# Performance work log

Measured on AMD Instinct MI355X. Metric: run time of the kernel, lower is better.

Reference implementation:

```python
import jax, jax.numpy as jnp
import numpy as np

SAMPLE_RATE = 22050
N_FFT = 1024
HOP = 256
K_HARM = 3


def _hann(n):
    # periodic hann window (torch.hann_window default)
    return 0.5 * (1.0 - jnp.cos(2.0 * jnp.pi * jnp.arange(n) / n))


def _stft(x, window):
    # x: (B, T) real -> (B, F, T') complex. Matches torchaudio Spectrogram
    # (center=True, reflect pad, power=None, normalized=False).
    pad = N_FFT // 2
    xp = jnp.pad(x, ((0, 0), (pad, pad)), mode='reflect')
    n_frames = 1 + (xp.shape[-1] - N_FFT) // HOP
    idx = jnp.arange(n_frames)[:, None] * HOP + jnp.arange(N_FFT)[None, :]
    frames = xp[:, idx] * window  # (B, T', n_fft)
    return jnp.fft.rfft(frames, axis=-1).transpose(0, 2, 1)  # (B, F, T')


def _resize_f(x, f_out):
    # bilinear resize along freq axis only (time size unchanged =>
    # reduces to 1D linear interp, align_corners=False semantics).
    f_in = x.shape[1]
    src = jnp.clip((jnp.arange(f_out) + 0.5) * (f_in / f_out) - 0.5, 0.0, f_in - 1.0)
    i0 = jnp.floor(src).astype(jnp.int32)
    i1 = jnp.minimum(i0 + 1, f_in - 1)
    w = (src - i0)[None, :, None]
    return x[:, i0] * (1.0 - w) + x[:, i1] * w


def _harmonic_plane(mag):
    # mag: (B, F, T). HPS in log domain.
    F = mag.shape[1]
    hs = jnp.log1p(mag)
    for k in range(2, K_HARM + 1):
        hs = hs + jnp.log1p(_resize_f(_resize_f(mag, F // k), F))
    return jnp.expm1(hs)[:, None]  # (B,1,F,T)


def _spread_matrix(F):
    freqs = jnp.linspace(0.0, SAMPLE_RATE / 2.0, F)
    bark = 13.0 * jnp.arctan(0.00076 * freqs) + 3.5 * jnp.arctan((freqs / 7500.0) ** 2)
    d = jnp.abs(bark[:, None] - bark[None, :])  # (F, F)
    mask = jnp.where(d <= 0.0,
                     jnp.exp(-0.5 * d ** 2),
                     jnp.exp(-0.7 * (d / 0.5) ** 2))
    return mask / (jnp.sum(mask, axis=1, keepdims=True) + 1e-8)


def _psychoacoustic_plane(mag):
    # mag: (B, F, T)
    F = mag.shape[1]
    mag = jnp.maximum(mag, 1e-10)
    mag_db = jnp.clip(20.0 * jnp.log10(mag), -100.0, 0.0)
    mag_db = (mag_db + 100.0) / 100.0
    spread = _spread_matrix(F)
    masking = jnp.einsum('fg,bgt->bft', spread, mag_db)  # batched GEMM replaces per-(b,t) loop
    return jnp.clip(masking - 0.12, 0.0, 1.0)[:, None]  # (B,1,F,T)


def _forward(waveform):
    # waveform: (B, 2, T) float32
    window = _hann(N_FFT).astype(waveform.dtype)
    spec_l = _stft(waveform[:, 0], window)  # (B,F,T') complex64
    spec_r = _stft(waveform[:, 1], window)
    spec = (spec_l + spec_r) / 2.0
    mag = jnp.abs(spec)  # (B,F,T')

    harmonic = _harmonic_plane(mag)

    ipd = jnp.angle(spec_l) - jnp.angle(spec_r)
    el = jnp.abs(spec_l) ** 2
    er = jnp.abs(spec_r) ** 2
    panning = (el - er) / (el + er + 1e-10)
    spatial = jnp.stack([ipd, panning], axis=1)  # (B,2,F,T')

    psy = _psychoacoustic_plane(mag)

    out = jnp.concatenate([spec.real[:, None], spec.imag[:, None],
                           harmonic, spatial, psy], axis=1)  # (B,6,F,T')
    return out


def setup_inputs() -> dict:
    key = jax.random.key(0)
    waveform = jax.random.normal(key, (8, 2, 661500), dtype=jnp.float32)
    return {"waveform": waveform}


def reference(waveform):
    return _forward(waveform)
```

## Files before the change

kernel.cpp:

```cpp
#include <hip/hip_runtime.h>
#include <math.h>

namespace {

constexpr int kB   = 8;
constexpr int kT   = 661500;
constexpr int kHop = 256;
constexpr int kNF  = 513;
constexpr int kNT  = 2584;
constexpr int kKP  = 544;
constexpr int kFP  = 576;
constexpr size_t kFT = (size_t)kNF * kNT;

constexpr size_t kDbBytes  = (size_t)kB * kNT * kKP * 2;
constexpr size_t kSbBytes  = (size_t)kFP * kKP * 2;
constexpr size_t kCstBytes = kDbBytes + kSbBytes;
typedef __attribute__((ext_vector_type(8))) short bf16x8;
typedef __attribute__((ext_vector_type(4))) float f32x4;

__device__ __forceinline__ int swz(int i) { return i ^ ((i >> 5) & 31); }

__device__ __forceinline__ ushort f2bf(float x) {
  unsigned u = __float_as_uint(x);
  return (ushort)((u + 0x7FFFu + ((u >> 16) & 1u)) >> 16);
}

__global__ __launch_bounds__(256) void k_const(float* __restrict__ cst) {
  const int tid = threadIdx.x;
  for (int j = tid; j < 512; j += 256) {
    float s, c;
    sincospif((float)j * (1.0f / 512.0f), &s, &c);
    cst[j] = c;
    cst[512 + j] = -s;
  }
  const float c2pi = 6.28318548202514648f;
  for (int n = tid; n < 1024; n += 256) {
    float arg = ((float)n * c2pi) * (1.0f / 1024.0f);
    cst[1024 + n] = 0.5f * (1.0f - cosf(arg));
  }
}

__global__ __launch_bounds__(256) void k_stft(const float* __restrict__ x,
                                              float* __restrict__ out,
                                              ushort* __restrict__ Db,
                                              const float* __restrict__ cst) {
  const int t = blockIdx.x;
  const int b = blockIdx.y;
  const int tid = threadIdx.x;
  __shared__ float sre[1024];
  __shared__ float sim[1024];
  __shared__ float twr[512];
  __shared__ float twi[512];
  __shared__ float mags[kNF];
  __shared__ float d2[256];
  __shared__ float d3[171];

  for (int j = tid; j < 512; j += 256) {
    twr[j] = cst[j];
    twi[j] = cst[512 + j];
  }

  const float* wtb = cst + 1024;
  const float* xb = x + (size_t)b * 2 * kT;
  const int start = t * kHop - 512;
  if (t >= 2 && t < kNT - 1) {
    const float4 l4 = ((const float4*)(xb + start))[tid];
    const float4 r4 = ((const float4*)(xb + kT + start))[tid];
    const float4 w4 = ((const float4*)wtb)[tid];
    float lv[4] = {l4.x * w4.x, l4.y * w4.y, l4.z * w4.z, l4.w * w4.w};
    float rw[4] = {r4.x * w4.x, r4.y * w4.y, r4.z * w4.z, r4.w * w4.w};
#pragma unroll
    for (int e = 0; e < 4; ++e) {
      int n = tid * 4 + e;
      int rv = (int)(__brev((unsigned)n) >> 22);
      int rs = swz(rv);
      sre[rs] = lv[e];
      sim[rs] = rw[e];
    }
  } else {
#pragma unroll
    for (int q = 0; q < 4; ++q) {
      int n = tid + q * 256;
      int g = start + n;
      g = (g < 0) ? -g : g;
      g = (g >= kT) ? (2 * kT - 2 - g) : g;
      float wv = wtb[n];
      float l = xb[g] * wv;
      float r = xb[(size_t)kT + g] * wv;
      int rv = (int)(__brev((unsigned)n) >> 22);
      int rs = swz(rv);
      sre[rs] = l;
      sim[rs] = r;
    }
  }
  __syncthreads();

#pragma unroll
  for (int s = 1; s <= 10; ++s) {
    const int half = 1 << (s - 1);
#pragma unroll
    for (int jj = 0; jj < 2; ++jj) {
      int j = tid + jj * 256;
      int pos = j & (half - 1);
      int i0 = ((j >> (s - 1)) << s) + pos;
      int i1 = i0 + half;
      int ti = pos << (10 - s);
      float wr = twr[ti], wi = twi[ti];
      int a0 = swz(i0), a1 = swz(i1);
      float xr = sre[a1], xi = sim[a1];
      float br = xr * wr - xi * wi;
      float bi = xr * wi + xi * wr;
      float cr = sre[a0], ci = sim[a0];
      sre[a0] = cr + br; sim[a0] = ci + bi;
      sre[a1] = cr - br; sim[a1] = ci - bi;
    }
    __syncthreads();
  }

  float* outb = out + (size_t)b * 6 * kFT;
  const size_t row = (size_t)t * kNF;
  float* pre = outb + 1 * kFT + row;
  float* pim = outb + 2 * kFT + row;
  float* phm = outb + 3 * kFT + row;
  float* pip = outb + 4 * kFT + row;
  float* ppn = outb + 5 * kFT + row;
  ushort* pdb = Db + ((size_t)b * kNT + t) * kKP;

  for (int k = tid; k < kNF; k += 256) {
    int k2 = (1024 - k) & 1023;
    float a = sre[swz(k)], bb = sim[swz(k)];
    float c = sre[swz(k2)], d = sim[swz(k2)];
    float Lre = 0.5f * (a + c), Lim = 0.5f * (bb - d);
    float Rre = 0.5f * (bb + d), Rim = 0.5f * (c - a);
    float sr = 0.5f * (Lre + Rre), si = 0.5f * (Lim + Rim);
    float mg = sqrtf(sr * sr + si * si);
    mags[k] = mg;
    float ipd = atan2f(Lim, Lre) - atan2f(Rim, Rre);
    float el = Lre * Lre + Lim * Lim;
    float er = Rre * Rre + Rim * Rim;
    float pan = (el - er) / (el + er + 1e-10f);
    float mm = fmaxf(mg, 1e-10f);
    float db = 20.0f * log10f(mm);
    db = fminf(fmaxf(db, -100.0f), 0.0f);
    pre[k] = sr;
    pim[k] = si;
    pip[k] = ipd;
    ppn[k] = pan;
    pdb[k] = f2bf((db + 100.0f) * 0.01f);
  }
  for (int k = kNF + tid; k < kKP; k += 256) pdb[k] = 0;
  __syncthreads();

  {
    int j = tid;
    float src = __fsub_rn(__fmul_rn((float)j + 0.5f, 513.0f / 256.0f), 0.5f);
    src = fminf(fmaxf(src, 0.0f), 512.0f);
    int i0 = (int)src;
    int i1 = min(i0 + 1, 512);
    float w = src - (float)i0;
    d2[j] = mags[i0] * (1.0f - w) + mags[i1] * w;
  }
  if (tid < 171) {
    int j = tid;
    float src = __fsub_rn(__fmul_rn((float)j + 0.5f, 3.0f), 0.5f);
    src = fminf(fmaxf(src, 0.0f), 512.0f);
    int i0 = (int)src;
    int i1 = min(i0 + 1, 512);
    float w = src - (float)i0;
    d3[j] = mags[i0] * (1.0f - w) + mags[i1] * w;
  }
  __syncthreads();

  for (int k = tid; k < kNF; k += 256) {
    float s2 = __fsub_rn(__fmul_rn((float)k + 0.5f, 256.0f / 513.0f), 0.5f);
    s2 = fminf(fmaxf(s2, 0.0f), 255.0f);
    int a0 = (int)s2;
    int a1 = min(a0 + 1, 255);
    float w2 = s2 - (float)a0;
    float u2 = d2[a0] * (1.0f - w2) + d2[a1] * w2;

    float s3 = __fsub_rn(__fmul_rn((float)k + 0.5f, 171.0f / 513.0f), 0.5f);
    s3 = fminf(fmaxf(s3, 0.0f), 170.0f);
    int c0 = (int)s3;
    int c1 = min(c0 + 1, 170);
    float w3 = s3 - (float)c0;
    float u3 = d3[c0] * (1.0f - w3) + d3[c1] * w3;

    float hs = log1pf(mags[k]) + log1pf(u2) + log1pf(u3);
    phm[k] = expm1f(hs);
  }
}

__global__ __launch_bounds__(256) void k_transpose(float* __restrict__ out, int c) {
  __shared__ float tile[64][65];
  const int t0 = blockIdx.x * 64;
  const int f0 = blockIdx.y * 64;
  const int b = blockIdx.z;
  const float* src = out + ((size_t)b * 6 + (c + 1)) * kFT;
  float* dst = out + ((size_t)b * 6 + c) * kFT;
  for (int i = threadIdx.x; i < 4096; i += 256) {
    int tl = i >> 6, fl = i & 63;
    int t = t0 + tl, f = f0 + fl;
    float v = 0.0f;
    if (t < kNT && f < kNF) v = src[(size_t)t * kNF + f];
    tile[fl][tl] = v;
  }
  __syncthreads();
  for (int i = threadIdx.x; i < 4096; i += 256) {
    int fl = i >> 6, tl = i & 63;
    int t = t0 + tl, f = f0 + fl;
    if (t < kNT && f < kNF)
      dst[(size_t)f * kNT + t] = tile[fl][tl];
  }
}

__global__ __launch_bounds__(256) void k_spread(ushort* __restrict__ Sb) {
  const int f = blockIdx.x;
  const int tid = threadIdx.x;
  ushort* rowp = Sb + (size_t)f * kKP;
  if (f >= kNF) {
    for (int g = tid; g < kKP; g += 256) rowp[g] = 0;
    return;
  }
  __shared__ float bark[kNF];
  __shared__ float rowv[kNF];
  __shared__ float red[256];
  for (int g = tid; g < kNF; g += 256) {
    float fr = (float)g * (11025.0f / 512.0f);
    float r = fr * (1.0f / 7500.0f);
    bark[g] = 13.0f * atanf(0.00076f * fr) + 3.5f * atanf(r * r);
  }
  __syncthreads();
  float bf = bark[f];
  float partial = 0.0f;
  for (int g = tid; g < kNF; g += 256) {
    float d = fabsf(bf - bark[g]);
    float v = expf(-2.8f * d * d);
    rowv[g] = v;
    partial += v;
  }
  red[tid] = partial;
  __syncthreads();
  for (int off = 128; off > 0; off >>= 1) {
    if (tid < off) red[tid] += red[tid + off];
    __syncthreads();
  }
  float inv = 1.0f / (red[0] + 1e-8f);
  for (int g = tid; g < kNF; g += 256) rowp[g] = f2bf(rowv[g] * inv);
  for (int g = kNF + tid; g < kKP; g += 256) rowp[g] = 0;
}

__global__ __launch_bounds__(256) void k_psy(const ushort* __restrict__ Sb,
                                             const ushort* __restrict__ Db,
                                             float* __restrict__ out) {
  const int tid = threadIdx.x;
  const int w = tid >> 6;
  const int l = tid & 63;
  const int lr = l & 15;
  const int lk = (l >> 4) * 8;
  const int f0 = blockIdx.y * 64 + w * 16;
  const int t0 = blockIdx.x * 64;
  const int b = blockIdx.z;

  const ushort* ap = Sb + (size_t)(f0 + lr) * kKP + lk;
  const size_t dbase = (size_t)b * kNT;
  const ushort* bp0 = Db + (dbase + min(t0 + lr,      kNT - 1)) * kKP + lk;
  const ushort* bp1 = Db + (dbase + min(t0 + lr + 16, kNT - 1)) * kKP + lk;
  const ushort* bp2 = Db + (dbase + min(t0 + lr + 32, kNT - 1)) * kKP + lk;
  const ushort* bp3 = Db + (dbase + min(t0 + lr + 48, kNT - 1)) * kKP + lk;

  f32x4 acc0 = {0.f, 0.f, 0.f, 0.f};
  f32x4 acc1 = {0.f, 0.f, 0.f, 0.f};
  f32x4 acc2 = {0.f, 0.f, 0.f, 0.f};
  f32x4 acc3 = {0.f, 0.f, 0.f, 0.f};
#pragma unroll 1
  for (int g0 = 0; g0 < kKP; g0 += 32) {
    bf16x8 a  = *(const bf16x8*)ap;  ap  += 32;
    bf16x8 b0 = *(const bf16x8*)bp0; bp0 += 32;
    bf16x8 b1 = *(const bf16x8*)bp1; bp1 += 32;
    bf16x8 b2 = *(const bf16x8*)bp2; bp2 += 32;
    bf16x8 b3 = *(const bf16x8*)bp3; bp3 += 32;
    acc0 = __builtin_amdgcn_mfma_f32_16x16x32_bf16(a, b0, acc0, 0, 0, 0);
    acc1 = __builtin_amdgcn_mfma_f32_16x16x32_bf16(a, b1, acc1, 0, 0, 0);
    acc2 = __builtin_amdgcn_mfma_f32_16x16x32_bf16(a, b2, acc2, 0, 0, 0);
    acc3 = __builtin_amdgcn_mfma_f32_16x16x32_bf16(a, b3, acc3, 0, 0, 0);
  }

  float* o5 = out + ((size_t)b * 6 + 5) * kFT;
  const int frow = f0 + (l >> 4) * 4;
  const int tcol = t0 + lr;
#pragma unroll
  for (int r = 0; r < 4; ++r) {
    int f = frow + r;
    if (f >= kNF) break;
    float vs[4] = {acc0[r], acc1[r], acc2[r], acc3[r]};
#pragma unroll
    for (int tt = 0; tt < 4; ++tt) {
      int t = tcol + 16 * tt;
      if (t < kNT) {
        float v = vs[tt] - 0.12f;
        v = fminf(fmaxf(v, 0.0f), 1.0f);
        o5[(size_t)f * kNT + t] = v;
      }
    }
  }
}

}

extern "C" void kernel_launch(void* const* d_in, const int* in_sizes, int n_in,
                              void* d_out, int out_size, void* d_ws, size_t ws_size,
                              hipStream_t stream) {
  const float* x = (const float*)d_in[0];
  float* out = (float*)d_out;
  ushort* Db = (ushort*)d_ws;
  ushort* Sb = (ushort*)((char*)d_ws + kDbBytes);
  float* cst = (float*)((char*)d_ws + kCstBytes);

  hipLaunchKernelGGL(k_const, dim3(1), dim3(256), 0, stream, cst);
  hipLaunchKernelGGL(k_spread, dim3(kFP), dim3(256), 0, stream, Sb);
  hipLaunchKernelGGL(k_stft, dim3(kNT, kB), dim3(256), 0, stream, x, out, Db, cst);
  for (int c = 0; c < 5; ++c) {
    hipLaunchKernelGGL(k_transpose, dim3((kNT + 63) / 64, (kNF + 63) / 64, kB),
                       dim3(256), 0, stream, out, c);
  }
  hipLaunchKernelGGL(k_psy, dim3((kNT + 63) / 64, (kFP + 63) / 64, kB),
                     dim3(256), 0, stream, Sb, Db, out);
}
```

Before: 657.4 us.

## Stage STFT outputs as bf16, use radix-4 FFT, fast math, retile psy GEMM

The STFT kernel now writes its intermediate per-frame channels as bf16 into packed scratch regions of the output. The transpose kernels read those bf16 values and handle several channels per launch, which halves intermediate traffic and cuts launches from five to three. The FFT moves from ten radix-2 passes to five radix-4 passes with a new LDS swizzle, so there are fewer barriers. atan2, log10, the divide and the log1p/expm1 chain are replaced by a polynomial atan2, log2, reciprocal and a product form. The psy GEMM is retiled so each wave shares one B fragment across four A rows. The cost is precision: bf16 rounding of real, imag, ipd, pan and harmonic outputs, plus the approximate transcendentals, may exceed output tolerances.

After: 573.0 us. 1.15x faster.

```diff
diff --git a/kernel.cpp b/kernel.cpp
--- a/kernel.cpp
+++ b/kernel.cpp
@@ -18,11 +18,26 @@
 typedef __attribute__((ext_vector_type(8))) short bf16x8;
 typedef __attribute__((ext_vector_type(4))) float f32x4;
 
-__device__ __forceinline__ int swz(int i) { return i ^ ((i >> 5) & 31); }
+__device__ __forceinline__ int swz(int i) { return i ^ (i >> 2); }
 
 __device__ __forceinline__ ushort f2bf(float x) {
   unsigned u = __float_as_uint(x);
   return (ushort)((u + 0x7FFFu + ((u >> 16) & 1u)) >> 16);
+}
+__device__ __forceinline__ float bf2f(ushort u) {
+  return __uint_as_float((unsigned)u << 16);
+}
+
+__device__ __forceinline__ float fatan2(float y, float x) {
+  float ax = fabsf(x), ay = fabsf(y);
+  float mx = fmaxf(ax, ay), mn = fminf(ax, ay);
+  float a = mn * __frcp_rn(fmaxf(mx, 1e-38f));
+  float s = a * a;
+  float r = fmaf(s, fmaf(s, fmaf(s, fmaf(s, fmaf(s, -0.0117212f, 0.05265332f),
+            -0.11643287f), 0.19354346f), -0.33262347f), 0.99997726f) * a;
+  if (ay > ax) r = 1.57079632679f - r;
+  if (x < 0.0f) r = 3.14159265359f - r;
+  return copysignf(r, y);
 }
 
 __global__ __launch_bounds__(256) void k_const(float* __restrict__ cst) {
@@ -63,19 +78,18 @@
   const float* wtb = cst + 1024;
   const float* xb = x + (size_t)b * 2 * kT;
   const int start = t * kHop - 512;
-  if (t >= 2 && t < kNT - 1) {
+  if (t >= 2 && t <= 2581) {
     const float4 l4 = ((const float4*)(xb + start))[tid];
     const float4 r4 = ((const float4*)(xb + kT + start))[tid];
     const float4 w4 = ((const float4*)wtb)[tid];
     float lv[4] = {l4.x * w4.x, l4.y * w4.y, l4.z * w4.z, l4.w * w4.w};
-    float rw[4] = {r4.x * w4.x, r4.y * w4.y, r4.z * w4.z, r4.w * w4.w};
+    float rv_[4] = {r4.x * w4.x, r4.y * w4.y, r4.z * w4.z, r4.w * w4.w};
 #pragma unroll
     for (int e = 0; e < 4; ++e) {
       int n = tid * 4 + e;
-      int rv = (int)(__brev((unsigned)n) >> 22);
-      int rs = swz(rv);
+      int rs = swz((int)(__brev((unsigned)n) >> 22));
       sre[rs] = lv[e];
-      sim[rs] = rw[e];
+      sim[rs] = rv_[e];
     }
   } else {
 #pragma unroll
@@ -85,45 +99,53 @@
       g = (g < 0) ? -g : g;
       g = (g >= kT) ? (2 * kT - 2 - g) : g;
       float wv = wtb[n];
-      float l = xb[g] * wv;
-      float r = xb[(size_t)kT + g] * wv;
-      int rv = (int)(__brev((unsigned)n) >> 22);
-      int rs = swz(rv);
-      sre[rs] = l;
-      sim[rs] = r;
-    }
-  }
-  __syncthreads();
-
-#pragma unroll
-  for (int s = 1; s <= 10; ++s) {
-    const int half = 1 << (s - 1);
-#pragma unroll
-    for (int jj = 0; jj < 2; ++jj) {
-      int j = tid + jj * 256;
-      int pos = j & (half - 1);
-      int i0 = ((j >> (s - 1)) << s) + pos;
-      int i1 = i0 + half;
-      int ti = pos << (10 - s);
-      float wr = twr[ti], wi = twi[ti];
-      int a0 = swz(i0), a1 = swz(i1);
-      float xr = sre[a1], xi = sim[a1];
-      float br = xr * wr - xi * wi;
-      float bi = xr * wi + xi * wr;
-      float cr = sre[a0], ci = sim[a0];
-      sre[a0] = cr + br; sim[a0] = ci + bi;
-      sre[a1] = cr - br; sim[a1] = ci - bi;
-    }
+      int rs = swz((int)(__brev((unsigned)n) >> 22));
+      sre[rs] = xb[g] * wv;
+      sim[rs] = xb[(size_t)kT + g] * wv;
+    }
+  }
+
+#pragma unroll
+  for (int p = 0; p < 5; ++p) {
     __syncthreads();
-  }
-
-  float* outb = out + (size_t)b * 6 * kFT;
+    const int half = 1 << (2 * p);
+    const int c1 = swz(half), c2s = swz(2 * half), c3s = swz(3 * half);
+    const int pos = tid & (half - 1);
+    const int i0 = ((tid >> (2 * p)) << (2 * p + 2)) + pos;
+    const int a0 = swz(i0), a1 = a0 ^ c1, a2 = a0 ^ c2s, a3 = a0 ^ c3s;
+    const int ti1 = pos << (9 - 2 * p);
+    const int ti2 = pos << (8 - 2 * p);
+    float w1r = twr[ti1], w1i = twi[ti1];
+    float w2r = twr[ti2], w2i = twi[ti2];
+    float e0r = sre[a0], e0i = sim[a0];
+    float e1r = sre[a1], e1i = sim[a1];
+    float e2r = sre[a2], e2i = sim[a2];
+    float e3r = sre[a3], e3i = sim[a3];
+    float t1r = e1r * w1r - e1i * w1i, t1i = e1r * w1i + e1i * w1r;
+    float t3r = e3r * w1r - e3i * w1i, t3i = e3r * w1i + e3i * w1r;
+    float u0r = e0r + t1r, u0i = e0i + t1i;
+    float u1r = e0r - t1r, u1i = e0i - t1i;
+    float u2r = e2r + t3r, u2i = e2i + t3i;
+    float u3r = e2r - t3r, u3i = e2i - t3i;
+    float q2r = u2r * w2r - u2i * w2i, q2i = u2r * w2i + u2i * w2r;
+    float q3r = u3r * w2r - u3i * w2i, q3i = u3r * w2i + u3i * w2r;
+    sre[a0] = u0r + q2r; sim[a0] = u0i + q2i;
+    sre[a2] = u0r - q2r; sim[a2] = u0i - q2i;
+    sre[a1] = u1r + q3i; sim[a1] = u1i - q3r;
+    sre[a3] = u1r - q3i; sim[a3] = u1i + q3r;
+  }
+  __syncthreads();
+
+  ushort* outU = (ushort*)out;
+  const size_t c2o = ((size_t)b * 6 + 2) * (2 * kFT);
+  const size_t c4o = ((size_t)b * 6 + 4) * (2 * kFT);
+  const size_t c5o = ((size_t)b * 6 + 5) * (2 * kFT);
   const size_t row = (size_t)t * kNF;
-  float* pre = outb + 1 * kFT + row;
-  float* pim = outb + 2 * kFT + row;
-  float* phm = outb + 3 * kFT + row;
-  float* pip = outb + 4 * kFT + row;
-  float* ppn = outb + 5 * kFT + row;
+  ushort* pre = outU + c2o + row;
+  ushort* pim = outU + c2o + kFT + row;
+  ushort* phm = outU + c4o + row;
+  ushort* pip = outU + c4o + kFT + row;
+  ushort* ppn = outU + c5o + row;
   ushort* pdb = Db + ((size_t)b * kNT + t) * kKP;
 
   for (int k = tid; k < kNF; k += 256) {
@@ -135,17 +157,17 @@
     float sr = 0.5f * (Lre + Rre), si = 0.5f * (Lim + Rim);
     float mg = sqrtf(sr * sr + si * si);
     mags[k] = mg;
-    float ipd = atan2f(Lim, Lre) - atan2f(Rim, Rre);
+    float ipd = fatan2(Lim, Lre) - fatan2(Rim, Rre);
     float el = Lre * Lre + Lim * Lim;
     float er = Rre * Rre + Rim * Rim;
-    float pan = (el - er) / (el + er + 1e-10f);
+    float pan = (el - er) * __frcp_rn(el + er + 1e-10f);
     float mm = fmaxf(mg, 1e-10f);
-    float db = 20.0f * log10f(mm);
+    float db = 6.02059991328f * __log2f(mm);
     db = fminf(fmaxf(db, -100.0f), 0.0f);
-    pre[k] = sr;
-    pim[k] = si;
-    pip[k] = ipd;
-    ppn[k] = pan;
+    pre[k] = f2bf(sr);
+    pim[k] = f2bf(si);
+    pip[k] = f2bf(ipd);
+    ppn[k] = f2bf(pan);
     pdb[k] = f2bf((db + 100.0f) * 0.01f);
   }
   for (int k = kNF + tid; k < kKP; k += 256) pdb[k] = 0;
@@ -186,31 +208,37 @@
     float w3 = s3 - (float)c0;
     float u3 = d3[c0] * (1.0f - w3) + d3[c1] * w3;
 
-    float hs = log1pf(mags[k]) + log1pf(u2) + log1pf(u3);
-    phm[k] = expm1f(hs);
-  }
-}
-
-__global__ __launch_bounds__(256) void k_transpose(float* __restrict__ out, int c) {
+    float hp = (1.0f + mags[k]) * (1.0f + u2) * (1.0f + u3) - 1.0f;
+    phm[k] = f2bf(hp);
+  }
+}
+
+__global__ __launch_bounds__(256) void k_transpose(float* __restrict__ out,
+                                                   int src_res, int dst_res0,
+                                                   int nch) {
   __shared__ float tile[64][65];
   const int t0 = blockIdx.x * 64;
   const int f0 = blockIdx.y * 64;
   const int b = blockIdx.z;
-  const float* src = out + ((size_t)b * 6 + (c + 1)) * kFT;
-  float* dst = out + ((size_t)b * 6 + c) * kFT;
-  for (int i = threadIdx.x; i < 4096; i += 256) {
-    int tl = i >> 6, fl = i & 63;
-    int t = t0 + tl, f = f0 + fl;
-    float v = 0.0f;
-    if (t < kNT && f < kNF) v = src[(size_t)t * kNF + f];
-    tile[fl][tl] = v;
-  }
-  __syncthreads();
-  for (int i = threadIdx.x; i < 4096; i += 256) {
-    int fl = i >> 6, tl = i & 63;
-    int t = t0 + tl, f = f0 + fl;
-    if (t < kNT && f < kNF)
-      dst[(size_t)f * kNT + t] = tile[fl][tl];
+  const ushort* sbase = (const ushort*)(out + ((size_t)b * 6 + src_res) * kFT);
+  for (int cc = 0; cc < nch; ++cc) {
+    const ushort* sp = sbase + (size_t)cc * kFT;
+    float* dst = out + ((size_t)b * 6 + dst_res0 + cc) * kFT;
+    for (int i = threadIdx.x; i < 4096; i += 256) {
+      int tl = i >> 6, fl = i & 63;
+      int t = t0 + tl, f = f0 + fl;
+      float v = 0.0f;
+      if (t < kNT && f < kNF) v = bf2f(sp[(size_t)t * kNF + f]);
+      tile[fl][tl] = v;
+    }
+    __syncthreads();
+    for (int i = threadIdx.x; i < 4096; i += 256) {
+      int fl = i >> 6, tl = i & 63;
+      int t = t0 + tl, f = f0 + fl;
+      if (t < kNT && f < kNF)
+        dst[(size_t)f * kNT + t] = tile[fl][tl];
+    }
+    __syncthreads();
   }
 }
 
@@ -258,16 +286,12 @@
   const int l = tid & 63;
   const int lr = l & 15;
   const int lk = (l >> 4) * 8;
-  const int f0 = blockIdx.y * 64 + w * 16;
-  const int t0 = blockIdx.x * 64;
+  const int f0 = blockIdx.y * 64;
+  const int t0 = blockIdx.x * 64 + w * 16;
   const int b = blockIdx.z;
 
   const ushort* ap = Sb + (size_t)(f0 + lr) * kKP + lk;
-  const size_t dbase = (size_t)b * kNT;
-  const ushort* bp0 = Db + (dbase + min(t0 + lr,      kNT - 1)) * kKP + lk;
-  const ushort* bp1 = Db + (dbase + min(t0 + lr + 16, kNT - 1)) * kKP + lk;
-  const ushort* bp2 = Db + (dbase + min(t0 + lr + 32, kNT - 1)) * kKP + lk;
-  const ushort* bp3 = Db + (dbase + min(t0 + lr + 48, kNT - 1)) * kKP + lk;
+  const ushort* bp = Db + ((size_t)b * kNT + min(t0 + lr, kNT - 1)) * kKP + lk;
 
   f32x4 acc0 = {0.f, 0.f, 0.f, 0.f};
   f32x4 acc1 = {0.f, 0.f, 0.f, 0.f};
@@ -275,32 +299,33 @@
   f32x4 acc3 = {0.f, 0.f, 0.f, 0.f};
 #pragma unroll 1
   for (int g0 = 0; g0 < kKP; g0 += 32) {
-    bf16x8 a  = *(const bf16x8*)ap;  ap  += 32;
-    bf16x8 b0 = *(const bf16x8*)bp0; bp0 += 32;
-    bf16x8 b1 = *(const bf16x8*)bp1; bp1 += 32;
-    bf16x8 b2 = *(const bf16x8*)bp2; bp2 += 32;
-    bf16x8 b3 = *(const bf16x8*)bp3; bp3 += 32;
-    acc0 = __builtin_amdgcn_mfma_f32_16x16x32_bf16(a, b0, acc0, 0, 0, 0);
-    acc1 = __builtin_amdgcn_mfma_f32_16x16x32_bf16(a, b1, acc1, 0, 0, 0);
-    acc2 = __builtin_amdgcn_mfma_f32_16x16x32_bf16(a, b2, acc2, 0, 0, 0);
-    acc3 = __builtin_amdgcn_mfma_f32_16x16x32_bf16(a, b3, acc3, 0, 0, 0);
+    bf16x8 bb = *(const bf16x8*)bp; bp += 32;
+    bf16x8 a0 = *(const bf16x8*)(ap);
+    bf16x8 a1 = *(const bf16x8*)(ap + 16 * kKP);
+    bf16x8 a2 = *(const bf16x8*)(ap + 32 * kKP);
+    bf16x8 a3 = *(const bf16x8*)(ap + 48 * kKP);
+    ap += 32;
+    acc0 = __builtin_amdgcn_mfma_f32_16x16x32_bf16(a0, bb, acc0, 0, 0, 0);
+    acc1 = __builtin_amdgcn_mfma_f32_16x16x32_bf16(a1, bb, acc1, 0, 0, 0);
+    acc2 = __builtin_amdgcn_mfma_f32_16x16x32_bf16(a2, bb, acc2, 0, 0, 0);
+    acc3 = __builtin_amdgcn_mfma_f32_16x16x32_bf16(a3, bb, acc3, 0, 0, 0);
   }
 
   float* o5 = out + ((size_t)b * 6 + 5) * kFT;
-  const int frow = f0 + (l >> 4) * 4;
   const int tcol = t0 + lr;
-#pragma unroll
-  for (int r = 0; r < 4; ++r) {
-    int f = frow + r;
-    if (f >= kNF) break;
-    float vs[4] = {acc0[r], acc1[r], acc2[r], acc3[r]};
-#pragma unroll
-    for (int tt = 0; tt < 4; ++tt) {
-      int t = tcol + 16 * tt;
-      if (t < kNT) {
-        float v = vs[tt] - 0.12f;
-        v = fminf(fmaxf(v, 0.0f), 1.0f);
-        o5[(size_t)f * kNT + t] = v;
+  const int fbase = f0 + (l >> 4) * 4;
+  if (tcol < kNT) {
+    const f32x4 accs[4] = {acc0, acc1, acc2, acc3};
+#pragma unroll
+    for (int ff = 0; ff < 4; ++ff) {
+#pragma unroll
+      for (int r = 0; r < 4; ++r) {
+        int f = fbase + ff * 16 + r;
+        if (f < kNF) {
+          float v = accs[ff][r] - 0.12f;
+          v = fminf(fmaxf(v, 0.0f), 1.0f);
+          o5[(size_t)f * kNT + tcol] = v;
+        }
       }
     }
   }
@@ -320,10 +345,12 @@
   hipLaunchKernelGGL(k_const, dim3(1), dim3(256), 0, stream, cst);
   hipLaunchKernelGGL(k_spread, dim3(kFP), dim3(256), 0, stream, Sb);
   hipLaunchKernelGGL(k_stft, dim3(kNT, kB), dim3(256), 0, stream, x, out, Db, cst);
-  for (int c = 0; c < 5; ++c) {
-    hipLaunchKernelGGL(k_transpose, dim3((kNT + 63) / 64, (kNF + 63) / 64, kB),
-                       dim3(256), 0, stream, out, c);
-  }
+  hipLaunchKernelGGL(k_transpose, dim3((kNT + 63) / 64, (kNF + 63) / 64, kB),
+                     dim3(256), 0, stream, out, 2, 0, 2);
+  hipLaunchKernelGGL(k_transpose, dim3((kNT + 63) / 64, (kNF + 63) / 64, kB),
+                     dim3(256), 0, stream, out, 4, 2, 2);
+  hipLaunchKernelGGL(k_transpose, dim3((kNT + 63) / 64, (kNF + 63) / 64, kB),
+                     dim3(256), 0, stream, out, 5, 4, 1);
   hipLaunchKernelGGL(k_psy, dim3((kNT + 63) / 64, (kFP + 63) / 64, kB),
                      dim3(256), 0, stream, Sb, Db, out);
 }
```
